# Kernel optimization log

Measured on AMD Instinct MI355X. Metric: run time of the kernel, lower is better.

Reference implementation:

```python
import jax, jax.numpy as jnp
import numpy as np

EPS = 1e-6
NS = 0.1  # negative_slope
BN_EPS = 1e-5
ZCA_EPS = 1e-5
NPOINT, K = 2048, 16


def fps(xyz, npoint):
    # deterministic farthest point sampling, start index 0 per batch
    B, N, _ = xyz.shape
    bidx = jnp.arange(B)
    def step(carry, _):
        distance, farthest = carry
        centroid = xyz[bidx, farthest]                    # (B,3)
        d = jnp.sum((xyz - centroid[:, None, :]) ** 2, axis=-1)
        distance = jnp.minimum(distance, d)
        return (distance, jnp.argmax(distance, axis=-1)), farthest
    init = (jnp.full((B, N), 1e10, xyz.dtype), jnp.zeros((B,), jnp.int32))
    _, idxs = jax.lax.scan(step, init, None, length=npoint)
    return idxs.T                                          # (B, npoint)


def knn(k, xyz, new_xyz):
    # squared euclidean distances give the same topk ordering as torch.cdist
    d2 = (jnp.sum(new_xyz ** 2, -1)[:, :, None]
          + jnp.sum(xyz ** 2, -1)[:, None, :]
          - 2.0 * jnp.einsum('bmd,bnd->bmn', new_xyz, xyz))
    _, idx = jax.lax.top_k(-d2, k)
    return idx                                             # (B, M, k)


def vn_sa(xyz, feat, W_feat, W_dir, bn_weight, bn_bias, gamma, fps_idx, group_idx):
    B, N, _ = xyz.shape
    C = feat.shape[1]
    M, k = group_idx.shape[1], group_idx.shape[2]
    new_xyz = jnp.take_along_axis(xyz, fps_idx[:, :, None], axis=1)          # (B,M,3)
    anchor = jnp.take_along_axis(feat, fps_idx[:, None, None, :], axis=3)    # (B,C,3,M)
    neigh_xyz = jnp.take_along_axis(xyz, group_idx.reshape(B, M * k, 1), axis=1).reshape(B, M, k, 3)
    rel = (neigh_xyz - new_xyz[:, :, None, :]).transpose(0, 3, 1, 2)[:, None]  # (B,1,3,M,k)
    neigh = jnp.take_along_axis(feat, group_idx.reshape(B, 1, 1, M * k), axis=3).reshape(B, C, 3, M, k)
    anchor_rep = jnp.broadcast_to(anchor[..., None], neigh.shape)
    edge = jnp.concatenate([neigh - anchor_rep, anchor_rep, rel], axis=1)    # (B,2C+1,3,M,k)
    # VNLinearLeakyReLU (dim=5) with VNBatchNorm (training-mode batch stats, affine=1/0)
    p = jnp.einsum('oc,bcvmk->bovmk', W_feat, edge)
    norm = jnp.linalg.norm(p, axis=2) + EPS                                  # (B,O,M,k)
    mu = norm.mean(axis=(0, 2, 3), keepdims=True)
    var = norm.var(axis=(0, 2, 3), keepdims=True)
    norm_bn = (norm - mu) / jnp.sqrt(var + BN_EPS) * bn_weight[None, :, None, None] + bn_bias[None, :, None, None]
    p = p / norm[:, :, None] * norm_bn[:, :, None]
    d = jnp.einsum('oc,bcvmk->bovmk', W_dir, edge)
    dot = jnp.sum(p * d, axis=2, keepdims=True)
    mask = (dot >= 0).astype(p.dtype)
    dsq = jnp.sum(d * d, axis=2, keepdims=True)
    h = NS * p + (1 - NS) * (mask * p + (1 - mask) * (p - dot / (dsq + EPS) * d))
    nf = h.mean(axis=-1)                                                     # (B,O,3,M) mean pool
    # VNZCALayerNorm
    O = nf.shape[1]
    xf = nf.transpose(0, 2, 1, 3).reshape(B, 3, -1).astype(jnp.float32)      # (B,3,O*M)
    xc = xf - xf.mean(axis=-1, keepdims=True)
    Mt = xc.shape[-1]
    cov = xc @ xc.transpose(0, 2, 1) / (float(Mt) + EPS) + ZCA_EPS * jnp.eye(3, dtype=xc.dtype)
    w, v = jnp.linalg.eigh(cov)
    w = jnp.maximum(w, ZCA_EPS)
    Wz = jnp.einsum('bij,bj,bkj->bik', v, 1.0 / jnp.sqrt(w), v)
    xw = (Wz @ xc).reshape(B, 3, O, M).transpose(0, 2, 1, 3).astype(nf.dtype)
    return new_xyz, xw * gamma


def setup_inputs():
    key = jax.random.key(0)
    ks = jax.random.split(key, 4)
    B, N, Cin, Cout = 4, 8192, 32, 64
    edge_in = 2 * Cin + 1
    return {
        'xyz': jax.random.normal(ks[0], (B, N, 3), jnp.float32),
        'feat': jax.random.normal(ks[1], (B, Cin, 3, N), jnp.float32),
        'W_feat': jax.random.normal(ks[2], (Cout, edge_in), jnp.float32) * 0.1,
        'W_dir': jax.random.normal(ks[3], (Cout, edge_in), jnp.float32) * 0.1,
        'bn_weight': jnp.ones((Cout,), jnp.float32),
        'bn_bias': jnp.zeros((Cout,), jnp.float32),
        'gamma': jnp.ones((1, Cout, 1, 1), jnp.float32),
    }


def reference(xyz, feat, W_feat, W_dir, bn_weight, bn_bias, gamma):
    fps_idx = fps(xyz, NPOINT)
    new_xyz = jnp.take_along_axis(xyz, fps_idx[:, :, None], axis=1)
    group_idx = knn(K, xyz, new_xyz)
    return vn_sa(xyz, feat, W_feat, W_dir, bn_weight, bn_bias, gamma, fps_idx, group_idx)
```

## Files before the change

### kernel.cpp

```cpp
#include <hip/hip_runtime.h>
#include <stdint.h>

#define DI __device__ __forceinline__

static constexpr int B   = 4;
static constexpr int N   = 8192;
static constexpr int M   = 2048;
static constexpr int KNN = 16;
static constexpr int O   = 64;
static constexpr int E   = 65;

typedef float f32x2 __attribute__((ext_vector_type(2)));

DI float fadd(float a, float b){ return __fadd_rn(a,b); }
DI float fsub(float a, float b){ return __fsub_rn(a,b); }
DI float fmul(float a, float b){ return __fmul_rn(a,b); }

template<int CTRL>
DI float dppmax(float v){
  int t = __builtin_amdgcn_update_dpp(0, __float_as_int(v), CTRL, 0xf, 0xf, true);
  return fmaxf(v, __int_as_float(t));
}

__global__ __launch_bounds__(256) void k_transpose(const float* __restrict__ feat,
                                                   float* __restrict__ featT){
  __shared__ float tile[64*97];
  int blk = blockIdx.x;
  int b = blk / (N/64);
  int n0 = (blk % (N/64)) * 64;
  const float* fb = feat + (size_t)b*96*N;
  for (int e = threadIdx.x; e < 96*64; e += 256){
    int cv = e >> 6, nn = e & 63;
    tile[nn*97 + cv] = fb[(size_t)cv*N + n0 + nn];
  }
  __syncthreads();
  float* ob = featT + ((size_t)b*N + n0)*96;
  for (int e = threadIdx.x; e < 96*64; e += 256){
    int nn = e / 96, cv = e - nn*96;
    ob[e] = tile[nn*97 + cv];
  }
}

__global__ __launch_bounds__(256) void k_xyz_pre(const float* __restrict__ xyz,
                                                 float* __restrict__ xsoa,
                                                 float* __restrict__ sx){
  int i = blockIdx.x*256 + threadIdx.x;
  if (i >= B*N) return;
  int b = i >> 13, n = i & 8191;
  float x = xyz[(size_t)i*3+0], y = xyz[(size_t)i*3+1], z = xyz[(size_t)i*3+2];
  xsoa[((size_t)b*3+0)*N + n] = x;
  xsoa[((size_t)b*3+1)*N + n] = y;
  xsoa[((size_t)b*3+2)*N + n] = z;
  sx[i] = fadd(fadd(fmul(x,x),fmul(y,y)),fmul(z,z));
}

__global__ __launch_bounds__(256, 1) void k_fps(const float* __restrict__ xsoa,
                                                int* __restrict__ fps_idx,
                                                float* __restrict__ newxyz){
  #pragma clang fp contract(off)
  int b = blockIdx.x;
  const float* X = xsoa + (size_t)b*3*N;
  __shared__ float lx[N], ly[N], lz[N];
  __shared__ uint2 swp[2][4];
  int tid = threadIdx.x;
  int lane = tid & 63;
  int wid = tid >> 6;

  for (int j = tid; j < N; j += 256){
    lx[j] = X[j]; ly[j] = X[N+j]; lz[j] = X[2*N+j];
  }
  __syncthreads();

  f32x2 px[16], py[16], pz[16], ds[16];
  const f32x2* lx2 = (const f32x2*)lx;
  const f32x2* ly2 = (const f32x2*)ly;
  const f32x2* lz2 = (const f32x2*)lz;
  #pragma unroll
  for (int i = 0; i < 16; ++i){
    px[i] = lx2[tid*16+i]; py[i] = ly2[tid*16+i]; pz[i] = lz2[tid*16+i];
    ds[i] = (f32x2){1e10f, 1e10f};
  }
  float cx = lx[0], cy = ly[0], cz = lz[0];
  if (tid == 0){
    fps_idx[b*M] = 0;
    newxyz[(size_t)(b*M)*3+0] = cx;
    newxyz[(size_t)(b*M)*3+1] = cy;
    newxyz[(size_t)(b*M)*3+2] = cz;
  }

  for (int it = 1; it < M; ++it){
    f32x2 c2x = (f32x2){cx,cx}, c2y = (f32x2){cy,cy}, c2z = (f32x2){cz,cz};
    float vmA = -1.f, vmB = -1.f;
    #pragma unroll
    for (int i = 0; i < 16; ++i){
      f32x2 dx = px[i] - c2x;
      f32x2 dy = py[i] - c2y;
      f32x2 dz = pz[i] - c2z;
      f32x2 s  = (dx*dx + dy*dy) + dz*dz;
      float nx = fminf(ds[i].x, s.x);
      float ny = fminf(ds[i].y, s.y);
      ds[i].x = nx; ds[i].y = ny;
      vmA = fmaxf(vmA, nx); vmB = fmaxf(vmB, ny);
    }
    float vmax = fmaxf(vmA, vmB);

    int fj = 0;
    #pragma unroll
    for (int i = 15; i >= 0; --i){
      if (ds[i].y == vmax) fj = 2*i+1;
      if (ds[i].x == vmax) fj = 2*i;
    }

    float t = vmax;
    t = dppmax<0xB1>(t);
    t = dppmax<0x4E>(t);
    t = dppmax<0x141>(t);
    t = dppmax<0x140>(t);
    t = dppmax<0x142>(t);
    t = dppmax<0x143>(t);
    float wm = __int_as_float(__builtin_amdgcn_readlane(__float_as_int(t), 63));

    unsigned long long mask = __ballot(vmax == wm);
    int firstlane = __ffsll(mask) - 1;
    int widx = __builtin_amdgcn_readlane(tid*32 + fj, firstlane);

    int buf = it & 1;
    if (lane == 0) swp[buf][wid] = make_uint2(__float_as_uint(wm), (unsigned)widx);
    __syncthreads();
    unsigned bv = swp[buf][0].x; int gi = (int)swp[buf][0].y;
    #pragma unroll
    for (int w_ = 1; w_ < 4; ++w_){
      unsigned vv = swp[buf][w_].x;
      if (vv > bv){ bv = vv; gi = (int)swp[buf][w_].y; }
    }
    cx = lx[gi]; cy = ly[gi]; cz = lz[gi];
    if (tid == 0){
      fps_idx[b*M+it] = gi;
      newxyz[(size_t)(b*M+it)*3+0] = cx;
      newxyz[(size_t)(b*M+it)*3+1] = cy;
      newxyz[(size_t)(b*M+it)*3+2] = cz;
    }
  }
}

__global__ __launch_bounds__(256) void k_knn(const float* __restrict__ xsoa,
                                             const float* __restrict__ sx,
                                             const float* __restrict__ newxyz,
                                             int* __restrict__ gidx){
  __shared__ unsigned long long heap[4][64][17];
  __shared__ unsigned long long outk[4][16];
  int tid = threadIdx.x;
  int lane = tid & 63, wv = tid >> 6;
  int w = blockIdx.x*4 + wv;
  int b = w >> 11;
  const float* X  = xsoa + (size_t)b*3*N;
  const float* SX = sx   + (size_t)b*N;
  float qx = newxyz[(size_t)w*3+0], qy = newxyz[(size_t)w*3+1], qz = newxyz[(size_t)w*3+2];
  float sn = fadd(fadd(fmul(qx,qx),fmul(qy,qy)),fmul(qz,qz));

  unsigned long long cand[16];
  #pragma unroll
  for (int i = 0; i < 16; ++i) cand[i] = 0xFFFFFFFFFFFFFFFFull;

  for (int r = 0; r < 128; ++r){
    int n = (r << 6) + lane;
    float p0 = fmul(qx, X[n]), p1 = fmul(qy, X[N+n]), p2 = fmul(qz, X[2*N+n]);
    float dot = fadd(fadd(p0, p1), p2);
    float d2  = fsub(fadd(sn, SX[n]), fmul(2.0f, dot));
    unsigned u = __float_as_uint(d2);
    u ^= ((unsigned)((int)u >> 31)) | 0x80000000u;
    unsigned long long key = ((unsigned long long)u << 32) | (unsigned)n;
    if (key < cand[15]){
      #pragma unroll
      for (int i = 0; i < 16; ++i){
        unsigned long long a = cand[i];
        bool sw = key < a;
        unsigned long long lo = sw ? key : a;
        unsigned long long hi = sw ? a : key;
        cand[i] = lo; key = hi;
      }
    }
  }
  #pragma unroll
  for (int i = 0; i < 16; ++i) heap[wv][lane][i] = cand[i];
  unsigned long long my = cand[0];
  int head = 0;
  for (int round = 0; round < 16; ++round){
    unsigned long long k = my;
    #pragma unroll
    for (int s = 1; s < 64; s <<= 1){
      unsigned long long o_ = __shfl_xor(k, s, 64);
      if (o_ < k) k = o_;
    }
    if (my == k){
      ++head;
      my = (head < 16) ? heap[wv][lane][head] : 0xFFFFFFFFFFFFFFFFull;
    }
    if (lane == 0) outk[wv][round] = k;
  }
  __syncthreads();
  if (lane < 16) gidx[(size_t)w*16 + lane] = (int)(unsigned)(outk[wv][lane] & 0xFFFFFFFFull);
}

template<int PASSB>
__global__ __launch_bounds__(256) void k_conv(const float* __restrict__ featT,
                                              const float* __restrict__ xsoa,
                                              const float* __restrict__ newxyz,
                                              const int*   __restrict__ fps_idx,
                                              const int*   __restrict__ gidx,
                                              const float* __restrict__ Wf,
                                              const float* __restrict__ Wd,
                                              const float* __restrict__ bn_stats,
                                              const float* __restrict__ bn_bias,
                                              float* __restrict__ bn_part,
                                              float* __restrict__ nf){
  __shared__ float sW0[O*E];
  __shared__ float sW1[PASSB ? O*E : 1];
  __shared__ __align__(16) float sNG[99*20];
  __shared__ float sA[96];
  __shared__ float red[3*256];

  int blk = blockIdx.x;
  int b = blk >> 11, m = blk & 2047;
  int tid = threadIdx.x;

  for (int e = tid; e < O*E; e += 256) sW0[e] = Wf[e];
  if (PASSB){ for (int e = tid; e < O*E; e += 256) sW1[e] = Wd[e]; }
  int aidx = fps_idx[blk];
  if (tid < 96) sA[tid] = featT[((size_t)(b*N) + aidx)*96 + tid];

  #pragma unroll 4
  for (int kk = 0; kk < KNN; ++kk){
    int n = gidx[(size_t)blk*KNN + kk];
    if (tid < 96){
      sNG[tid*20 + kk] = featT[((size_t)(b*N) + n)*96 + tid];
    } else if (tid < 99){
      int v = tid - 96;
      sNG[(96+v)*20 + kk] = fsub(xsoa[((size_t)(b*3+v))*N + n], newxyz[(size_t)blk*3 + v]);
    }
  }
  __syncthreads();

  int o  = tid & 63;
  int w0 = tid >> 6;

  float awf[3] = {0,0,0}, awd[3] = {0,0,0};
  for (int c = 0; c < 32; ++c){
    float df = sW0[o*E+32+c] - sW0[o*E+c];
    float dd = PASSB ? (sW1[o*E+32+c] - sW1[o*E+c]) : 0.f;
    #pragma unroll
    for (int v = 0; v < 3; ++v){
      float a = sA[c*3+v];
      awf[v] = fmaf(df, a, awf[v]);
      if (PASSB) awd[v] = fmaf(dd, a, awd[v]);
    }
  }

  float p[4][3], q[4][3];
  {
    float wr  = sW0[o*E+64];
    float wrd = PASSB ? sW1[o*E+64] : 0.f;
    #pragma unroll
    for (int v = 0; v < 3; ++v){
      const float4 rv = *reinterpret_cast<const float4*>(&sNG[(96+v)*20 + 4*w0]);
      const float* rp = reinterpret_cast<const float*>(&rv);
      #pragma unroll
      for (int r = 0; r < 4; ++r){
        p[r][v] = fmaf(wr, rp[r], awf[v]);
        q[r][v] = PASSB ? fmaf(wrd, rp[r], awd[v]) : 0.f;
      }
    }
  }
  for (int c = 0; c < 32; ++c){
    float wf = sW0[o*E+c];
    float wd = PASSB ? sW1[o*E+c] : 0.f;
    #pragma unroll
    for (int v = 0; v < 3; ++v){
      const float4 ev = *reinterpret_cast<const float4*>(&sNG[(c*3+v)*20 + 4*w0]);
      const float* ep = reinterpret_cast<const float*>(&ev);
      #pragma unroll
      for (int r = 0; r < 4; ++r){
        p[r][v] = fmaf(wf, ep[r], p[r][v]);
        if (PASSB) q[r][v] = fmaf(wd, ep[r], q[r][v]);
      }
    }
  }

  if (!PASSB){
    float s = 0.f, s2 = 0.f;
    #pragma unroll
    for (int r = 0; r < 4; ++r){
      float nrm = fadd(sqrtf(fadd(fadd(fmul(p[r][0],p[r][0]),fmul(p[r][1],p[r][1])),fmul(p[r][2],p[r][2]))), 1e-6f);
      s  = fadd(s, nrm);
      s2 = fadd(s2, fmul(nrm,nrm));
    }
    red[tid] = s; red[256+tid] = s2;
    __syncthreads();
    if (tid < 64){
      float a  = ((red[tid]    +red[tid+64])    +red[tid+128])    +red[tid+192];
      float a2 = ((red[256+tid]+red[256+tid+64])+red[256+tid+128])+red[256+tid+192];
      bn_part[(size_t)blk*128 + tid]      = a;
      bn_part[(size_t)blk*128 + 64 + tid] = a2;
    }
  } else {
    float mu = bn_stats[o], sc = bn_stats[64+o], bb = bn_bias[o];
    float hs[3] = {0.f,0.f,0.f};
    #pragma unroll
    for (int r = 0; r < 4; ++r){
      float nrm = fadd(sqrtf(fadd(fadd(fmul(p[r][0],p[r][0]),fmul(p[r][1],p[r][1])),fmul(p[r][2],p[r][2]))), 1e-6f);
      float nb  = fadd(fmul(fsub(nrm, mu), sc), bb);
      float rn  = nb / nrm;
      float pn0 = fmul(p[r][0], rn), pn1 = fmul(p[r][1], rn), pn2 = fmul(p[r][2], rn);
      float dot = fadd(fadd(fmul(pn0,q[r][0]),fmul(pn1,q[r][1])),fmul(pn2,q[r][2]));
      float dsq = fadd(fadd(fmul(q[r][0],q[r][0]),fmul(q[r][1],q[r][1])),fmul(q[r][2],q[r][2]));
      float t   = dot / fadd(dsq, 1e-6f);
      bool pos  = (dot >= 0.f);
      float pns[3] = {pn0, pn1, pn2};
      #pragma unroll
      for (int v = 0; v < 3; ++v){
        float inner = pos ? pns[v] : fsub(pns[v], fmul(t, q[r][v]));
        float h = fadd(fmul(0.1f, pns[v]), fmul(0.9f, inner));
        hs[v] = fadd(hs[v], h);
      }
    }
    red[tid] = hs[0]; red[256+tid] = hs[1]; red[512+tid] = hs[2];
    __syncthreads();
    if (tid < 64){
      #pragma unroll
      for (int v = 0; v < 3; ++v){
        const float* rv = red + v*256;
        float tot = ((rv[tid]+rv[tid+64])+rv[tid+128])+rv[tid+192];
        nf[(((size_t)(b*64+o))*3 + v)*M + m] = fmul(tot, 0.0625f);
      }
    }
  }
}

__global__ __launch_bounds__(256) void k_bnstats(const float* __restrict__ bn_part,
                                                 const float* __restrict__ bnw,
                                                 float* __restrict__ bn_stats){
  __shared__ float r1[256], r2[256];
  int o = blockIdx.x, tid = threadIdx.x;
  float s = 0.f, s2 = 0.f;
  for (int i = tid; i < B*M; i += 256){
    s  += bn_part[(size_t)i*128 + o];
    s2 += bn_part[(size_t)i*128 + 64 + o];
  }
  r1[tid] = s; r2[tid] = s2;
  __syncthreads();
  for (int off = 128; off > 0; off >>= 1){
    if (tid < off){ r1[tid] += r1[tid+off]; r2[tid] += r2[tid+off]; }
    __syncthreads();
  }
  if (tid == 0){
    float cnt = (float)(B*M*KNN);
    float mu  = r1[0] / cnt;
    float var = r2[0]/cnt - mu*mu;
    if (var < 0.f) var = 0.f;
    bn_stats[o]    = mu;
    bn_stats[64+o] = bnw[o] / sqrtf(var + 1e-5f);
  }
}

__global__ __launch_bounds__(1024) void k_zca(const float* __restrict__ nf,
                                              float* __restrict__ zca){
  int b = blockIdx.x, tid = threadIdx.x;
  double s1[3] = {0,0,0}, s2[6] = {0,0,0,0,0,0};
  for (int i = tid; i < O*M; i += 1024){
    int o = i >> 11, m = i & 2047;
    const float* base = nf + (((size_t)(b*O+o))*3)*M + m;
    double x = (double)base[0], y = (double)base[M], z = (double)base[2*M];
    s1[0]+=x;   s1[1]+=y;   s1[2]+=z;
    s2[0]+=x*x; s2[1]+=x*y; s2[2]+=x*z; s2[3]+=y*y; s2[4]+=y*z; s2[5]+=z*z;
  }
  #pragma unroll
  for (int s = 1; s < 64; s <<= 1){
    #pragma unroll
    for (int j = 0; j < 3; ++j) s1[j] += __shfl_xor(s1[j], s, 64);
    #pragma unroll
    for (int j = 0; j < 6; ++j) s2[j] += __shfl_xor(s2[j], s, 64);
  }
  __shared__ double red[16][9];
  int wid = tid >> 6, lane = tid & 63;
  if (lane == 0){
    red[wid][0]=s1[0]; red[wid][1]=s1[1]; red[wid][2]=s1[2];
    for (int j = 0; j < 6; ++j) red[wid][3+j] = s2[j];
  }
  __syncthreads();
  if (tid == 0){
    double S1[3]={0,0,0}, S2[6]={0,0,0,0,0,0};
    for (int w_ = 0; w_ < 16; ++w_){
      S1[0]+=red[w_][0]; S1[1]+=red[w_][1]; S1[2]+=red[w_][2];
      for (int j = 0; j < 6; ++j) S2[j]+=red[w_][3+j];
    }
    double Mt = (double)(O*M);
    double denom = Mt + 1e-6;
    double A[3][3];
    A[0][0]=(S2[0]-S1[0]*S1[0]/Mt)/denom + 1e-5;
    A[0][1]=A[1][0]=(S2[1]-S1[0]*S1[1]/Mt)/denom;
    A[0][2]=A[2][0]=(S2[2]-S1[0]*S1[2]/Mt)/denom;
    A[1][1]=(S2[3]-S1[1]*S1[1]/Mt)/denom + 1e-5;
    A[1][2]=A[2][1]=(S2[4]-S1[1]*S1[2]/Mt)/denom;
    A[2][2]=(S2[5]-S1[2]*S1[2]/Mt)/denom + 1e-5;
    double V[3][3]={{1,0,0},{0,1,0},{0,0,1}};
    for (int sweep = 0; sweep < 30; ++sweep){
      double offd = fabs(A[0][1])+fabs(A[0][2])+fabs(A[1][2]);
      if (offd < 1e-15) break;
      for (int pi = 0; pi < 3; ++pi) for (int qi = pi+1; qi < 3; ++qi){
        double apq = A[pi][qi];
        if (fabs(apq) < 1e-18) continue;
        double app = A[pi][pi], aqq = A[qi][qi];
        double theta = (aqq - app)/(2.0*apq);
        double t = ((theta >= 0) ? 1.0 : -1.0)/(fabs(theta) + sqrt(theta*theta + 1.0));
        double cth = 1.0/sqrt(t*t + 1.0), sth = t*cth;
        for (int r_ = 0; r_ < 3; ++r_){
          double arp=A[r_][pi], arq=A[r_][qi];
          A[r_][pi]=cth*arp - sth*arq;
          A[r_][qi]=sth*arp + cth*arq;
        }
        for (int c_ = 0; c_ < 3; ++c_){
          double apc=A[pi][c_], aqc=A[qi][c_];
          A[pi][c_]=cth*apc - sth*aqc;
          A[qi][c_]=sth*apc + cth*aqc;
        }
        for (int r_ = 0; r_ < 3; ++r_){
          double vrp=V[r_][pi], vrq=V[r_][qi];
          V[r_][pi]=cth*vrp - sth*vrq;
          V[r_][qi]=sth*vrp + cth*vrq;
        }
      }
    }
    double wv[3] = {A[0][0], A[1][1], A[2][2]};
    for (int j = 0; j < 3; ++j) if (wv[j] < 1e-5) wv[j] = 1e-5;
    double is[3] = {1.0/sqrt(wv[0]), 1.0/sqrt(wv[1]), 1.0/sqrt(wv[2])};
    for (int i = 0; i < 3; ++i)
      for (int j = 0; j < 3; ++j){
        double wz = V[i][0]*is[0]*V[j][0] + V[i][1]*is[1]*V[j][1] + V[i][2]*is[2]*V[j][2];
        zca[b*12 + i*3 + j] = (float)wz;
      }
    for (int j = 0; j < 3; ++j) zca[b*12 + 9 + j] = (float)(S1[j]/Mt);
  }
}

__global__ __launch_bounds__(256) void k_out(const float* __restrict__ nf,
                                             const float* __restrict__ zca,
                                             const float* __restrict__ gamma,
                                             float* __restrict__ out){
  int i = blockIdx.x*256 + threadIdx.x;
  if (i >= B*O*M) return;
  int m = i & 2047;
  int bo = i >> 11;
  int o = bo & 63;
  int b = bo >> 6;
  const float* W  = zca + b*12;
  const float* mn = W + 9;
  const float* base = nf + (size_t)bo*3*M + m;
  float c0 = fsub(base[0],   mn[0]);
  float c1 = fsub(base[M],   mn[1]);
  float c2 = fsub(base[2*M], mn[2]);
  float g = gamma[o];
  #pragma unroll
  for (int v = 0; v < 3; ++v){
    float val = fadd(fadd(fmul(W[v*3+0], c0), fmul(W[v*3+1], c1)), fmul(W[v*3+2], c2));
    out[(size_t)bo*3*M + (size_t)v*M + m] = fmul(val, g);
  }
}

extern "C" void kernel_launch(void* const* d_in, const int* in_sizes, int n_in,
                              void* d_out, int out_size, void* d_ws, size_t ws_size,
                              hipStream_t stream){
  const float* xyz  = (const float*)d_in[0];
  const float* feat = (const float*)d_in[1];
  const float* Wf   = (const float*)d_in[2];
  const float* Wd   = (const float*)d_in[3];
  const float* bnw  = (const float*)d_in[4];
  const float* bnb  = (const float*)d_in[5];
  const float* gam  = (const float*)d_in[6];
  float* out      = (float*)d_out;
  float* newxyz   = out;
  float* conv_out = out + (size_t)B*M*3;

  char* ws = (char*)d_ws;
  size_t off = 0;
  auto alloc = [&](size_t bytes)->void*{
    void* p = ws + off;
    off = (off + bytes + 255) & ~(size_t)255;
    return p;
  };
  float* featT    = (float*)alloc((size_t)B*N*96*4);
  float* xsoa     = (float*)alloc((size_t)B*3*N*4);
  float* sx       = (float*)alloc((size_t)B*N*4);
  int*   fpsi     = (int*)  alloc((size_t)B*M*4);
  int*   gidx     = (int*)  alloc((size_t)B*M*KNN*4);
  float* bn_part  = (float*)alloc((size_t)B*M*128*4);
  float* bn_stats = (float*)alloc(128*4);
  float* nf       = (float*)alloc((size_t)B*O*3*M*4);
  float* zca      = (float*)alloc(B*12*4);

  hipLaunchKernelGGL(k_transpose, dim3(B*(N/64)), dim3(256), 0, stream, feat, featT);
  hipLaunchKernelGGL(k_xyz_pre,   dim3(B*N/256),  dim3(256), 0, stream, xyz, xsoa, sx);
  hipLaunchKernelGGL(k_fps,       dim3(B),        dim3(256), 0, stream, xsoa, fpsi, newxyz);
  hipLaunchKernelGGL(k_knn,       dim3(B*M/4),    dim3(256), 0, stream, xsoa, sx, newxyz, gidx);
  hipLaunchKernelGGL((k_conv<0>), dim3(B*M),      dim3(256), 0, stream,
                     featT, xsoa, newxyz, fpsi, gidx, Wf, Wd, bn_stats, bnb, bn_part, nf);
  hipLaunchKernelGGL(k_bnstats,   dim3(O),        dim3(256), 0, stream, bn_part, bnw, bn_stats);
  hipLaunchKernelGGL((k_conv<1>), dim3(B*M),      dim3(256), 0, stream,
                     featT, xsoa, newxyz, fpsi, gidx, Wf, Wd, bn_stats, bnb, bn_part, nf);
  hipLaunchKernelGGL(k_zca,       dim3(B),        dim3(1024),0, stream, nf, zca);
  hipLaunchKernelGGL(k_out,       dim3((B*O*M)/256), dim3(256), 0, stream, nf, zca, gam, conv_out);
}
```

Measured before the change: 2.349 ms.

## Shorten FPS iteration critical path and transpose BN partial sums layout

The FPS inner loop now emits packed f32 sub/mul/add through inline asm, keeping the arithmetic unfused and paired. The winning lane of each wave now writes its candidate coordinates and max distance to shared memory, so after the barrier every thread picks the centroid directly instead of doing a readlane and a dependent LDS gather. The BN partial-sum buffer is stored channel-major so the stats reduction reads contiguously. Tie-breaking changes to the first wave holding the max, and comparing floats instead of uint bits should give the same order for non-negative distances.

```diff
diff --git a/kernel.cpp b/kernel.cpp
--- a/kernel.cpp
+++ b/kernel.cpp
@@ -20,6 +20,22 @@
 DI float dppmax(float v){
   int t = __builtin_amdgcn_update_dpp(0, __float_as_int(v), CTRL, 0xf, 0xf, true);
   return fmaxf(v, __int_as_float(t));
+}
+
+DI f32x2 pk_sub(f32x2 a, f32x2 b){
+  f32x2 d;
+  asm("v_pk_add_f32 %0, %1, %2 neg_lo:[0,1] neg_hi:[0,1]" : "=v"(d) : "v"(a), "v"(b));
+  return d;
+}
+DI f32x2 pk_mul(f32x2 a, f32x2 b){
+  f32x2 d;
+  asm("v_pk_mul_f32 %0, %1, %2" : "=v"(d) : "v"(a), "v"(b));
+  return d;
+}
+DI f32x2 pk_add(f32x2 a, f32x2 b){
+  f32x2 d;
+  asm("v_pk_add_f32 %0, %1, %2" : "=v"(d) : "v"(a), "v"(b));
+  return d;
 }
 
 __global__ __launch_bounds__(256) void k_transpose(const float* __restrict__ feat,
@@ -61,7 +77,8 @@
   int b = blockIdx.x;
   const float* X = xsoa + (size_t)b*3*N;
   __shared__ float lx[N], ly[N], lz[N];
-  __shared__ uint2 swp[2][4];
+  __shared__ float4   swpA[2][4];
+  __shared__ unsigned swpI[2][4];
   int tid = threadIdx.x;
   int lane = tid & 63;
   int wid = tid >> 6;
@@ -93,10 +110,13 @@
     float vmA = -1.f, vmB = -1.f;
     #pragma unroll
     for (int i = 0; i < 16; ++i){
-      f32x2 dx = px[i] - c2x;
-      f32x2 dy = py[i] - c2y;
-      f32x2 dz = pz[i] - c2z;
-      f32x2 s  = (dx*dx + dy*dy) + dz*dz;
+      f32x2 dx = pk_sub(px[i], c2x);
+      f32x2 dy = pk_sub(py[i], c2y);
+      f32x2 dz = pk_sub(pz[i], c2z);
+      f32x2 xx = pk_mul(dx, dx);
+      f32x2 yy = pk_mul(dy, dy);
+      f32x2 zz = pk_mul(dz, dz);
+      f32x2 s  = pk_add(pk_add(xx, yy), zz);
       float nx = fminf(ds[i].x, s.x);
       float ny = fminf(ds[i].y, s.y);
       ds[i].x = nx; ds[i].y = ny;
@@ -122,20 +142,23 @@
 
     unsigned long long mask = __ballot(vmax == wm);
     int firstlane = __ffsll(mask) - 1;
-    int widx = __builtin_amdgcn_readlane(tid*32 + fj, firstlane);
 
     int buf = it & 1;
-    if (lane == 0) swp[buf][wid] = make_uint2(__float_as_uint(wm), (unsigned)widx);
+    if (lane == firstlane){
+      int pi = tid*32 + fj;
+      float wx = lx[pi], wy = ly[pi], wz = lz[pi];
+      swpA[buf][wid] = make_float4(wx, wy, wz, vmax);
+      swpI[buf][wid] = (unsigned)pi;
+    }
     __syncthreads();
-    unsigned bv = swp[buf][0].x; int gi = (int)swp[buf][0].y;
-    #pragma unroll
-    for (int w_ = 1; w_ < 4; ++w_){
-      unsigned vv = swp[buf][w_].x;
-      if (vv > bv){ bv = vv; gi = (int)swp[buf][w_].y; }
-    }
-    cx = lx[gi]; cy = ly[gi]; cz = lz[gi];
+    float4   c0 = swpA[buf][0], c1 = swpA[buf][1], c2v = swpA[buf][2], c3 = swpA[buf][3];
+    unsigned i0 = swpI[buf][0], i1 = swpI[buf][1], i2 = swpI[buf][2], i3 = swpI[buf][3];
+    if (c1.w  > c0.w){ c0 = c1;  i0 = i1; }
+    if (c2v.w > c0.w){ c0 = c2v; i0 = i2; }
+    if (c3.w  > c0.w){ c0 = c3;  i0 = i3; }
+    cx = c0.x; cy = c0.y; cz = c0.z;
     if (tid == 0){
-      fps_idx[b*M+it] = gi;
+      fps_idx[b*M+it] = (int)i0;
       newxyz[(size_t)(b*M+it)*3+0] = cx;
       newxyz[(size_t)(b*M+it)*3+1] = cy;
       newxyz[(size_t)(b*M+it)*3+2] = cz;
@@ -299,8 +322,8 @@
     if (tid < 64){
       float a  = ((red[tid]    +red[tid+64])    +red[tid+128])    +red[tid+192];
       float a2 = ((red[256+tid]+red[256+tid+64])+red[256+tid+128])+red[256+tid+192];
-      bn_part[(size_t)blk*128 + tid]      = a;
-      bn_part[(size_t)blk*128 + 64 + tid] = a2;
+      bn_part[(size_t)tid*(B*M) + blk]        = a;
+      bn_part[(size_t)(64+tid)*(B*M) + blk]   = a2;
     }
   } else {
     float mu = bn_stats[o], sc = bn_stats[64+o], bb = bn_bias[o];
@@ -343,8 +366,8 @@
   int o = blockIdx.x, tid = threadIdx.x;
   float s = 0.f, s2 = 0.f;
   for (int i = tid; i < B*M; i += 256){
-    s  += bn_part[(size_t)i*128 + o];
-    s2 += bn_part[(size_t)i*128 + 64 + o];
+    s  += bn_part[(size_t)o*(B*M) + i];
+    s2 += bn_part[(size_t)(64+o)*(B*M) + i];
   }
   r1[tid] = s; r2[tid] = s2;
   __syncthreads();
```

Measured after the change: 3.197 ms. 36.1% more time.

## Vectorize FPS and edge-conv math, cache winner coords, transpose BN partials and nf

Applied to the files above, without the earlier changes.

In FPS, the min/max loop switches to packed f32x2 elementwise ops, and the winning lane writes its point's coordinates and max into shared memory. Other threads then read the centroid directly instead of re-indexing lx/ly/lz after the barrier. The edge-conv pass B uses packed f32x2 FMAs. The BN partials and the nf intermediate are stored in transposed layouts so the bnstats, zca and output kernels read them coalesced, and zca loads pairs. These are several independent micro-optimizations spread across different kernels.

```diff
diff --git a/kernel.cpp b/kernel.cpp
--- a/kernel.cpp
+++ b/kernel.cpp
@@ -15,6 +15,19 @@
 DI float fadd(float a, float b){ return __fadd_rn(a,b); }
 DI float fsub(float a, float b){ return __fsub_rn(a,b); }
 DI float fmul(float a, float b){ return __fmul_rn(a,b); }
+
+#if __has_builtin(__builtin_elementwise_min)
+DI f32x2 emin2(f32x2 a, f32x2 b){ return __builtin_elementwise_min(a,b); }
+DI f32x2 emax2(f32x2 a, f32x2 b){ return __builtin_elementwise_max(a,b); }
+#else
+DI f32x2 emin2(f32x2 a, f32x2 b){ return (f32x2){fminf(a.x,b.x), fminf(a.y,b.y)}; }
+DI f32x2 emax2(f32x2 a, f32x2 b){ return (f32x2){fmaxf(a.x,b.x), fmaxf(a.y,b.y)}; }
+#endif
+#if __has_builtin(__builtin_elementwise_fma)
+DI f32x2 efma(f32x2 a, f32x2 b, f32x2 c){ return __builtin_elementwise_fma(a,b,c); }
+#else
+DI f32x2 efma(f32x2 a, f32x2 b, f32x2 c){ return (f32x2){fmaf(a.x,b.x,c.x), fmaf(a.y,b.y,c.y)}; }
+#endif
 
 template<int CTRL>
 DI float dppmax(float v){
@@ -61,7 +74,8 @@
   int b = blockIdx.x;
   const float* X = xsoa + (size_t)b*3*N;
   __shared__ float lx[N], ly[N], lz[N];
-  __shared__ uint2 swp[2][4];
+  __shared__ float4   swpA[2][4];
+  __shared__ unsigned swpI[2][4];
   int tid = threadIdx.x;
   int lane = tid & 63;
   int wid = tid >> 6;
@@ -87,22 +101,22 @@
     newxyz[(size_t)(b*M)*3+1] = cy;
     newxyz[(size_t)(b*M)*3+2] = cz;
   }
+  int base = tid*32;
 
   for (int it = 1; it < M; ++it){
     f32x2 c2x = (f32x2){cx,cx}, c2y = (f32x2){cy,cy}, c2z = (f32x2){cz,cz};
-    float vmA = -1.f, vmB = -1.f;
+    f32x2 vm2 = (f32x2){-1.f,-1.f};
     #pragma unroll
     for (int i = 0; i < 16; ++i){
       f32x2 dx = px[i] - c2x;
       f32x2 dy = py[i] - c2y;
       f32x2 dz = pz[i] - c2z;
       f32x2 s  = (dx*dx + dy*dy) + dz*dz;
-      float nx = fminf(ds[i].x, s.x);
-      float ny = fminf(ds[i].y, s.y);
-      ds[i].x = nx; ds[i].y = ny;
-      vmA = fmaxf(vmA, nx); vmB = fmaxf(vmB, ny);
-    }
-    float vmax = fmaxf(vmA, vmB);
+      f32x2 nd = emin2(ds[i], s);
+      ds[i] = nd;
+      vm2 = emax2(vm2, nd);
+    }
+    float vmax = fmaxf(vm2.x, vm2.y);
 
     int fj = 0;
     #pragma unroll
@@ -122,20 +136,22 @@
 
     unsigned long long mask = __ballot(vmax == wm);
     int firstlane = __ffsll(mask) - 1;
-    int widx = __builtin_amdgcn_readlane(tid*32 + fj, firstlane);
 
     int buf = it & 1;
-    if (lane == 0) swp[buf][wid] = make_uint2(__float_as_uint(wm), (unsigned)widx);
+    if (lane == firstlane){
+      int pi = base + fj;
+      swpA[buf][wid] = make_float4(lx[pi], ly[pi], lz[pi], vmax);
+      swpI[buf][wid] = (unsigned)pi;
+    }
     __syncthreads();
-    unsigned bv = swp[buf][0].x; int gi = (int)swp[buf][0].y;
-    #pragma unroll
-    for (int w_ = 1; w_ < 4; ++w_){
-      unsigned vv = swp[buf][w_].x;
-      if (vv > bv){ bv = vv; gi = (int)swp[buf][w_].y; }
-    }
-    cx = lx[gi]; cy = ly[gi]; cz = lz[gi];
+    float4   s0 = swpA[buf][0], s1 = swpA[buf][1], s2v = swpA[buf][2], s3 = swpA[buf][3];
+    unsigned i0 = swpI[buf][0], i1 = swpI[buf][1], i2 = swpI[buf][2], i3 = swpI[buf][3];
+    if (s1.w  > s0.w){ s0 = s1;  i0 = i1; }
+    if (s2v.w > s0.w){ s0 = s2v; i0 = i2; }
+    if (s3.w  > s0.w){ s0 = s3;  i0 = i3; }
+    cx = s0.x; cy = s0.y; cz = s0.z;
     if (tid == 0){
-      fps_idx[b*M+it] = gi;
+      fps_idx[b*M+it] = (int)i0;
       newxyz[(size_t)(b*M+it)*3+0] = cx;
       newxyz[(size_t)(b*M+it)*3+1] = cy;
       newxyz[(size_t)(b*M+it)*3+2] = cz;
@@ -257,31 +273,56 @@
   }
 
   float p[4][3], q[4][3];
-  {
-    float wr  = sW0[o*E+64];
-    float wrd = PASSB ? sW1[o*E+64] : 0.f;
+  if (PASSB){
+    f32x2 pA[2][3], qA[2][3];
+    {
+      float wr  = sW0[o*E+64];
+      float wrd = sW1[o*E+64];
+      f32x2 wr2  = (f32x2){wr, wr};
+      f32x2 wrd2 = (f32x2){wrd, wrd};
+      #pragma unroll
+      for (int v = 0; v < 3; ++v){
+        const float4 rv = *reinterpret_cast<const float4*>(&sNG[(96+v)*20 + 4*w0]);
+        f32x2 r01 = (f32x2){rv.x, rv.y}, r23 = (f32x2){rv.z, rv.w};
+        f32x2 awf2 = (f32x2){awf[v], awf[v]};
+        f32x2 awd2 = (f32x2){awd[v], awd[v]};
+        pA[0][v] = efma(wr2,  r01, awf2);  pA[1][v] = efma(wr2,  r23, awf2);
+        qA[0][v] = efma(wrd2, r01, awd2);  qA[1][v] = efma(wrd2, r23, awd2);
+      }
+    }
+    for (int c = 0; c < 32; ++c){
+      float wf = sW0[o*E+c], wd = sW1[o*E+c];
+      f32x2 wf2 = (f32x2){wf, wf}, wd2 = (f32x2){wd, wd};
+      #pragma unroll
+      for (int v = 0; v < 3; ++v){
+        const float4 ev = *reinterpret_cast<const float4*>(&sNG[(c*3+v)*20 + 4*w0]);
+        f32x2 e01 = (f32x2){ev.x, ev.y}, e23 = (f32x2){ev.z, ev.w};
+        pA[0][v] = efma(wf2, e01, pA[0][v]);  pA[1][v] = efma(wf2, e23, pA[1][v]);
+        qA[0][v] = efma(wd2, e01, qA[0][v]);  qA[1][v] = efma(wd2, e23, qA[1][v]);
+      }
+    }
+    #pragma unroll
+    for (int v = 0; v < 3; ++v){
+      p[0][v] = pA[0][v].x; p[1][v] = pA[0][v].y; p[2][v] = pA[1][v].x; p[3][v] = pA[1][v].y;
+      q[0][v] = qA[0][v].x; q[1][v] = qA[0][v].y; q[2][v] = qA[1][v].x; q[3][v] = qA[1][v].y;
+    }
+  } else {
+    float wr = sW0[o*E+64];
     #pragma unroll
     for (int v = 0; v < 3; ++v){
       const float4 rv = *reinterpret_cast<const float4*>(&sNG[(96+v)*20 + 4*w0]);
       const float* rp = reinterpret_cast<const float*>(&rv);
       #pragma unroll
-      for (int r = 0; r < 4; ++r){
-        p[r][v] = fmaf(wr, rp[r], awf[v]);
-        q[r][v] = PASSB ? fmaf(wrd, rp[r], awd[v]) : 0.f;
-      }
-    }
-  }
-  for (int c = 0; c < 32; ++c){
-    float wf = sW0[o*E+c];
-    float wd = PASSB ? sW1[o*E+c] : 0.f;
-    #pragma unroll
-    for (int v = 0; v < 3; ++v){
-      const float4 ev = *reinterpret_cast<const float4*>(&sNG[(c*3+v)*20 + 4*w0]);
-      const float* ep = reinterpret_cast<const float*>(&ev);
-      #pragma unroll
-      for (int r = 0; r < 4; ++r){
-        p[r][v] = fmaf(wf, ep[r], p[r][v]);
-        if (PASSB) q[r][v] = fmaf(wd, ep[r], q[r][v]);
+      for (int r = 0; r < 4; ++r) p[r][v] = fmaf(wr, rp[r], awf[v]);
+    }
+    for (int c = 0; c < 32; ++c){
+      float wf = sW0[o*E+c];
+      #pragma unroll
+      for (int v = 0; v < 3; ++v){
+        const float4 ev = *reinterpret_cast<const float4*>(&sNG[(c*3+v)*20 + 4*w0]);
+        const float* ep = reinterpret_cast<const float*>(&ev);
+        #pragma unroll
+        for (int r = 0; r < 4; ++r) p[r][v] = fmaf(wf, ep[r], p[r][v]);
       }
     }
   }
@@ -299,8 +340,8 @@
     if (tid < 64){
       float a  = ((red[tid]    +red[tid+64])    +red[tid+128])    +red[tid+192];
       float a2 = ((red[256+tid]+red[256+tid+64])+red[256+tid+128])+red[256+tid+192];
-      bn_part[(size_t)blk*128 + tid]      = a;
-      bn_part[(size_t)blk*128 + 64 + tid] = a2;
+      bn_part[(size_t)tid*(B*M) + blk]        = a;
+      bn_part[(size_t)(64+tid)*(B*M) + blk]   = a2;
     }
   } else {
     float mu = bn_stats[o], sc = bn_stats[64+o], bb = bn_bias[o];
@@ -330,7 +371,7 @@
       for (int v = 0; v < 3; ++v){
         const float* rv = red + v*256;
         float tot = ((rv[tid]+rv[tid+64])+rv[tid+128])+rv[tid+192];
-        nf[(((size_t)(b*64+o))*3 + v)*M + m] = fmul(tot, 0.0625f);
+        nf[(((size_t)(b*3+v))*O + tid)*M + m] = fmul(tot, 0.0625f);
       }
     }
   }
@@ -343,8 +384,8 @@
   int o = blockIdx.x, tid = threadIdx.x;
   float s = 0.f, s2 = 0.f;
   for (int i = tid; i < B*M; i += 256){
-    s  += bn_part[(size_t)i*128 + o];
-    s2 += bn_part[(size_t)i*128 + 64 + o];
+    s  += bn_part[(size_t)o*(B*M) + i];
+    s2 += bn_part[(size_t)(64+o)*(B*M) + i];
   }
   r1[tid] = s; r2[tid] = s2;
   __syncthreads();
@@ -365,13 +406,18 @@
 __global__ __launch_bounds__(1024) void k_zca(const float* __restrict__ nf,
                                               float* __restrict__ zca){
   int b = blockIdx.x, tid = threadIdx.x;
+  const f32x2* xp = (const f32x2*)(nf + ((size_t)(b*3+0))*O*M);
+  const f32x2* yp = (const f32x2*)(nf + ((size_t)(b*3+1))*O*M);
+  const f32x2* zp = (const f32x2*)(nf + ((size_t)(b*3+2))*O*M);
   double s1[3] = {0,0,0}, s2[6] = {0,0,0,0,0,0};
-  for (int i = tid; i < O*M; i += 1024){
-    int o = i >> 11, m = i & 2047;
-    const float* base = nf + (((size_t)(b*O+o))*3)*M + m;
-    double x = (double)base[0], y = (double)base[M], z = (double)base[2*M];
-    s1[0]+=x;   s1[1]+=y;   s1[2]+=z;
-    s2[0]+=x*x; s2[1]+=x*y; s2[2]+=x*z; s2[3]+=y*y; s2[4]+=y*z; s2[5]+=z*z;
+  for (int i = tid; i < O*M/2; i += 1024){
+    f32x2 xv = xp[i], yv = yp[i], zv = zp[i];
+    #pragma unroll
+    for (int h = 0; h < 2; ++h){
+      double x = (double)xv[h], y = (double)yv[h], z = (double)zv[h];
+      s1[0]+=x;   s1[1]+=y;   s1[2]+=z;
+      s2[0]+=x*x; s2[1]+=x*y; s2[2]+=x*z; s2[3]+=y*y; s2[4]+=y*z; s2[5]+=z*z;
+    }
   }
   #pragma unroll
   for (int s = 1; s < 64; s <<= 1){
@@ -454,10 +500,10 @@
   int b = bo >> 6;
   const float* W  = zca + b*12;
   const float* mn = W + 9;
-  const float* base = nf + (size_t)bo*3*M + m;
-  float c0 = fsub(base[0],   mn[0]);
-  float c1 = fsub(base[M],   mn[1]);
-  float c2 = fsub(base[2*M], mn[2]);
+  size_t planeO = (size_t)O*M;
+  float c0 = fsub(nf[((size_t)(b*3+0))*planeO + (size_t)o*M + m], mn[0]);
+  float c1 = fsub(nf[((size_t)(b*3+1))*planeO + (size_t)o*M + m], mn[1]);
+  float c2 = fsub(nf[((size_t)(b*3+2))*planeO + (size_t)o*M + m], mn[2]);
   float g = gamma[o];
   #pragma unroll
   for (int v = 0; v < 3; ++v){
```

Measured after the change: 3.089 ms. +31.5%, slower.
